# Kernel optimization log

Measured on AMD Instinct MI355X. Metric: run time of the kernel, lower is better.

## Reference

```python
import jax, jax.numpy as jnp
import numpy as np

TAU_M, TAU_S = 4.0, 1.0
EM = float(np.exp(-1.0 / TAU_M))  # membrane decay exp(-1/tau_m)
ES = float(np.exp(-1.0 / TAU_S))  # synapse decay exp(-1/tau_s)
V_TH = 1.0


@jax.custom_vjp
def spike(v):
    # Heaviside spike with rectangular surrogate gradient (snn-iir style)
    return (v >= V_TH).astype(v.dtype)

def _spike_fwd(v):
    return spike(v), v

def _spike_bwd(v, g):
    return (g * (jnp.abs(v - V_TH) < 0.5).astype(g.dtype),)

spike.defvjp(_spike_fwd, _spike_bwd)


def dual_exp_iir(x, em, es):
    # dual-exponential synaptic filter as two coupled first-order IIRs
    # x: [B, F, T] -> y: [B, F, T]
    xT = jnp.moveaxis(x, -1, 0)  # [T, B, F]
    def step(carry, xt):
        m, s = carry
        m = em * m + xt
        s = es * s + xt
        return (m, s), m - s
    z = jnp.zeros_like(xT[0])
    _, y = jax.lax.scan(step, (z, z), xT)
    return jnp.moveaxis(y, 0, -1)


def lif_layer(x, w, b, decay):
    # Linear then LIF neuron with hard reset and membrane filter
    # x: [B, I, T], w: [O, I], b: [O] -> spikes: [B, O, T]
    wx = jnp.einsum('bit,oi->tbo', x, w) + b  # [T, B, O]
    def step(carry, cur):
        v, sp = carry
        v = decay * v * (1.0 - sp) + cur
        sp = spike(v)
        return (v, sp), sp
    z = jnp.zeros(wx.shape[1:], wx.dtype)
    _, spikes = jax.lax.scan(step, (z, z), wx)
    return jnp.moveaxis(spikes, 0, -1)


def setup_inputs() -> dict:
    key = jax.random.key(0)
    ks = jax.random.split(key, 8)
    B, T, F = 64, 512, 500
    inputs = jax.random.uniform(ks[0], (B, 784, T), jnp.float32)
    eps = jax.random.normal(ks[1], (B, F, T), jnp.float32)
    w1 = jax.random.normal(ks[2], (1000, 784), jnp.float32) * (1.0 / np.sqrt(784.0))
    b1 = jax.random.normal(ks[3], (1000,), jnp.float32) * 0.01
    w2 = jax.random.normal(ks[4], (500, 500), jnp.float32) * (1.0 / np.sqrt(500.0))
    b2 = jax.random.normal(ks[5], (500,), jnp.float32) * 0.01
    w3 = jax.random.normal(ks[6], (10, 500), jnp.float32) * (1.0 / np.sqrt(500.0))
    b3 = jax.random.normal(ks[7], (10,), jnp.float32) * 0.01
    return dict(inputs=inputs, eps=eps, w1=w1, b1=b1, w2=w2, b2=b2, w3=w3, b3=b3)


def reference(inputs, eps, w1, b1, w2, b2, w3, b3):
    F = 500
    # ANN encoder applied independently per timestep (steady_state)
    ann = jax.nn.relu(jnp.einsum('bit,oi->bot', inputs, w1) + b1[None, :, None])  # [B,1000,T]
    mu = ann[:, :F, :]
    ln_var = ann[:, F:, :]
    sample = mu + eps * jnp.exp(0.5 * ln_var)  # VAE reparameterization, [B,500,T]
    a2 = dual_exp_iir(sample, EM, ES)
    s2 = lif_layer(a2, w2, b2, EM)
    a3 = dual_exp_iir(s2, EM, ES)
    s3 = lif_layer(a3, w3, b3, EM)  # [B,10,T]
    return s3
```

## Files before the change

### kernel.cpp

```cpp
#include <hip/hip_runtime.h>

#define EMD 0.77880078307140486824
#define ESD 0.36787944117144232160
#define TCG 256
#define TCS 128

typedef double d4 __attribute__((ext_vector_type(4)));

__global__ void mfma_probe(double* __restrict__ flagOut)
{
    const int lane = threadIdx.x & 63;
    const int lr = lane & 15;
    const int lk = lane >> 4;
    const double a = 100.0 * lr + lk + 1.0;
    const double b = 1000.0 * lk + lr + 7.0;
    d4 c = {};
    c = __builtin_amdgcn_mfma_f64_16x16x4f64(a, b, c, 0, 0, 0);
    int myflag = 4;
    for (int h = 3; h >= 0; --h) {
        int ok = 1;
        for (int v = 0; v < 4; ++v) {
            int i, j;
            if (h == 0)      { i = 4 * lk + v; j = lr; }
            else if (h == 1) { i = lk + 4 * v; j = lr; }
            else if (h == 2) { i = lr; j = 4 * lk + v; }
            else             { i = lr; j = lk + 4 * v; }
            double e = 0.0;
            for (int k = 0; k < 4; ++k)
                e += (100.0 * i + k + 1.0) * (1000.0 * k + j + 7.0);
            if (c[v] != e) ok = 0;
        }
        if (__all(ok)) myflag = h;
    }
    if (lane == 0) flagOut[0] = (double)myflag;
}

__device__ __forceinline__ void frag_rc(int flag, int lk, int lr, int v,
                                        int& rl, int& cl)
{
    if (flag == 1)      { rl = lk + 4 * v; cl = lr; }
    else if (flag == 2) { rl = lr; cl = 4 * lk + v; }
    else if (flag == 3) { rl = lr; cl = lk + 4 * v; }
    else                { rl = 4 * lk + v; cl = lr; }
}

__global__ __launch_bounds__(256) void g1_mfma(
    const float* __restrict__ X,
    const float* __restrict__ W1,
    const float* __restrict__ B1,
    const float* __restrict__ EPS,
    double* __restrict__ SAMP,
    const double* __restrict__ FLG,
    int t0)
{
    const int b   = blockIdx.z;
    const int m0  = blockIdx.y * 64;
    const int tt0 = blockIdx.x * 64;
    const int tg  = t0 + tt0;

    __shared__ float Am[16][68];
    __shared__ float Al[16][68];
    __shared__ float Bs[16][68];

    const int tid  = threadIdx.x;
    const int lane = tid & 63;
    const int wid  = tid >> 6;
    const int wf   = (wid >> 1) * 32;
    const int wt   = (wid & 1) * 32;
    const int lr   = lane & 15;
    const int lk   = lane >> 4;

    d4 accm[2][2] = {};
    d4 accl[2][2] = {};

    for (int k0 = 0; k0 < 784; k0 += 16) {
        {
            const int m  = tid >> 2;
            const int kk = (tid & 3) * 4;
            int f = m0 + m; if (f > 499) f = 499;
            const float4 aw = *(const float4*)&W1[(size_t)f * 784 + k0 + kk];
            Am[kk+0][m] = aw.x; Am[kk+1][m] = aw.y;
            Am[kk+2][m] = aw.z; Am[kk+3][m] = aw.w;
            const float4 lw = *(const float4*)&W1[(size_t)(500 + f) * 784 + k0 + kk];
            Al[kk+0][m] = lw.x; Al[kk+1][m] = lw.y;
            Al[kk+2][m] = lw.z; Al[kk+3][m] = lw.w;
        }
        {
            const int bk = tid >> 4;
            const int bt = (tid & 15) * 4;
            *(float4*)&Bs[bk][bt] =
                *(const float4*)&X[((size_t)b * 784 + k0 + bk) * 512 + tg + bt];
        }
        __syncthreads();
        #pragma unroll
        for (int ks = 0; ks < 4; ++ks) {
            const int kr = 4 * ks + lk;
            const double a0 = (double)Am[kr][wf + lr];
            const double a1 = (double)Am[kr][wf + 16 + lr];
            const double l0 = (double)Al[kr][wf + lr];
            const double l1 = (double)Al[kr][wf + 16 + lr];
            const double b0 = (double)Bs[kr][wt + lr];
            const double b1 = (double)Bs[kr][wt + 16 + lr];
            accm[0][0] = __builtin_amdgcn_mfma_f64_16x16x4f64(a0, b0, accm[0][0], 0, 0, 0);
            accm[0][1] = __builtin_amdgcn_mfma_f64_16x16x4f64(a0, b1, accm[0][1], 0, 0, 0);
            accm[1][0] = __builtin_amdgcn_mfma_f64_16x16x4f64(a1, b0, accm[1][0], 0, 0, 0);
            accm[1][1] = __builtin_amdgcn_mfma_f64_16x16x4f64(a1, b1, accm[1][1], 0, 0, 0);
            accl[0][0] = __builtin_amdgcn_mfma_f64_16x16x4f64(l0, b0, accl[0][0], 0, 0, 0);
            accl[0][1] = __builtin_amdgcn_mfma_f64_16x16x4f64(l0, b1, accl[0][1], 0, 0, 0);
            accl[1][0] = __builtin_amdgcn_mfma_f64_16x16x4f64(l1, b0, accl[1][0], 0, 0, 0);
            accl[1][1] = __builtin_amdgcn_mfma_f64_16x16x4f64(l1, b1, accl[1][1], 0, 0, 0);
        }
        __syncthreads();
    }

    const int flag = (int)FLG[0];
    for (int fi = 0; fi < 2; ++fi)
    for (int tj = 0; tj < 2; ++tj)
    for (int v = 0; v < 4; ++v) {
        int rl, cl;
        frag_rc(flag, lk, lr, v, rl, cl);
        const int f = m0 + wf + fi * 16 + rl;
        if (f >= 500) continue;
        const int tloc = tt0 + wt + tj * 16 + cl;
        const double bm = (double)B1[f];
        const double bl = (double)B1[500 + f];
        const double mu = fmax(accm[fi][tj][v] + bm, 0.0);
        const double lv = fmax(accl[fi][tj][v] + bl, 0.0);
        const double e  = (double)EPS[((size_t)b * 500 + f) * 512 + t0 + tloc];
        SAMP[((size_t)b * 500 + f) * TCG + tloc] = mu + e * exp(0.5 * lv);
    }
}

__global__ __launch_bounds__(256) void iir2_chunk(
    double* __restrict__ A,
    double* __restrict__ stM, double* __restrict__ stS, int first)
{
    __shared__ double tile[64][65];
    const int tid = threadIdx.x;
    const int r0 = blockIdx.x * 64;
    double m = 0.0, s = 0.0;
    if (tid < 64 && !first) { m = stM[r0 + tid]; s = stS[r0 + tid]; }

    for (int sub = 0; sub < TCG / 64; ++sub) {
        #pragma unroll
        for (int q = 0; q < 8; ++q) {
            const int e2 = q * 256 + tid;
            const int r = e2 >> 5;
            const int c = (e2 & 31) * 2;
            const double2 v = *(const double2*)&A[(size_t)(r0 + r) * TCG + sub * 64 + c];
            tile[r][c] = v.x; tile[r][c + 1] = v.y;
        }
        __syncthreads();
        if (tid < 64) {
            #pragma unroll
            for (int c = 0; c < 64; ++c) {
                const double x = tile[tid][c];
                m = EMD * m + x;
                s = ESD * s + x;
                tile[tid][c] = m - s;
            }
        }
        __syncthreads();
        #pragma unroll
        for (int q = 0; q < 8; ++q) {
            const int e2 = q * 256 + tid;
            const int r = e2 >> 5;
            const int c = (e2 & 31) * 2;
            double2 v; v.x = tile[r][c]; v.y = tile[r][c + 1];
            *(double2*)&A[(size_t)(r0 + r) * TCG + sub * 64 + c] = v;
        }
        __syncthreads();
    }
    if (tid < 64) { stM[r0 + tid] = m; stS[r0 + tid] = s; }
}

__global__ __launch_bounds__(256) void g2_mfma(
    const double* __restrict__ A2,
    const float* __restrict__ W2,
    const float* __restrict__ B2,
    double* __restrict__ WX2,
    const double* __restrict__ FLG,
    int t_off)
{
    const int b   = blockIdx.z;
    const int o0  = blockIdx.y * 64;
    const int tl0 = blockIdx.x * 64;

    __shared__ double At[16][66];
    __shared__ float  Wo[16][68];

    const int tid  = threadIdx.x;
    const int lane = tid & 63;
    const int wid  = tid >> 6;
    const int wtl  = (wid >> 1) * 32;
    const int wo   = (wid & 1) * 32;
    const int lr   = lane & 15;
    const int lk   = lane >> 4;

    d4 acc[2][2] = {};

    for (int k0 = 0; k0 < 512; k0 += 16) {
        {
            const int kk = tid >> 4;
            const int t4 = (tid & 15) * 4;
            const int f = k0 + kk;
            if (f < 500) {
                const size_t base = ((size_t)b * 500 + f) * TCG + t_off + tl0 + t4;
                const double2 v0 = *(const double2*)&A2[base];
                const double2 v1 = *(const double2*)&A2[base + 2];
                At[kk][t4+0] = v0.x; At[kk][t4+1] = v0.y;
                At[kk][t4+2] = v1.x; At[kk][t4+3] = v1.y;
            } else {
                At[kk][t4+0] = 0.0; At[kk][t4+1] = 0.0;
                At[kk][t4+2] = 0.0; At[kk][t4+3] = 0.0;
            }
        }
        {
            const int oo = tid >> 2;
            const int fc = (tid & 3) * 4;
            int o = o0 + oo; if (o > 499) o = 499;
            const int f = k0 + fc;
            if (f + 3 < 500) {
                const float4 w = *(const float4*)&W2[(size_t)o * 500 + f];
                Wo[fc+0][oo] = w.x; Wo[fc+1][oo] = w.y;
                Wo[fc+2][oo] = w.z; Wo[fc+3][oo] = w.w;
            } else {
                #pragma unroll
                for (int c = 0; c < 4; ++c)
                    Wo[fc+c][oo] = (f + c < 500) ? W2[(size_t)o * 500 + f + c] : 0.0f;
            }
        }
        __syncthreads();
        #pragma unroll
        for (int ks = 0; ks < 4; ++ks) {
            const int kr = 4 * ks + lk;
            const double a0 = At[kr][wtl + lr];
            const double a1 = At[kr][wtl + 16 + lr];
            const double w0 = (double)Wo[kr][wo + lr];
            const double w1 = (double)Wo[kr][wo + 16 + lr];
            acc[0][0] = __builtin_amdgcn_mfma_f64_16x16x4f64(a0, w0, acc[0][0], 0, 0, 0);
            acc[0][1] = __builtin_amdgcn_mfma_f64_16x16x4f64(a0, w1, acc[0][1], 0, 0, 0);
            acc[1][0] = __builtin_amdgcn_mfma_f64_16x16x4f64(a1, w0, acc[1][0], 0, 0, 0);
            acc[1][1] = __builtin_amdgcn_mfma_f64_16x16x4f64(a1, w1, acc[1][1], 0, 0, 0);
        }
        __syncthreads();
    }

    const int flag = (int)FLG[0];
    for (int ti = 0; ti < 2; ++ti)
    for (int oj = 0; oj < 2; ++oj)
    for (int v = 0; v < 4; ++v) {
        int rl, cl;
        frag_rc(flag, lk, lr, v, rl, cl);
        const int tl = tl0 + wtl + ti * 16 + rl;
        const int o  = o0 + wo + oj * 16 + cl;
        if (o < 500)
            WX2[((size_t)tl * 64 + b) * 500 + o] = acc[ti][oj][v] + (double)B2[o];
    }
}

__global__ __launch_bounds__(256) void lif2iir3_chunk(
    double* __restrict__ WX,
    double* __restrict__ stV, double* __restrict__ stSp,
    double* __restrict__ stM, double* __restrict__ stS, int first)
{
    const int idx = blockIdx.x * 256 + threadIdx.x;
    if (idx >= 32000) return;
    double v, sp, m, s;
    if (first) { v = 0.0; sp = 0.0; m = 0.0; s = 0.0; }
    else { v = stV[idx]; sp = stSp[idx]; m = stM[idx]; s = stS[idx]; }
    for (int tt = 0; tt < TCS; ++tt) {
        const double cur = WX[(size_t)tt * 32000 + idx];
        v = EMD * v * (1.0 - sp) + cur;
        sp = (v >= 1.0) ? 1.0 : 0.0;
        m = EMD * m + sp;
        s = ESD * s + sp;
        WX[(size_t)tt * 32000 + idx] = m - s;
    }
    stV[idx] = v; stSp[idx] = sp; stM[idx] = m; stS[idx] = s;
}

__global__ __launch_bounds__(256) void g3_chunk(
    const double* __restrict__ A3,
    const float* __restrict__ W3,
    const float* __restrict__ B3,
    double* __restrict__ WX3)
{
    __shared__ float w3s[5000];
    for (int i = threadIdx.x; i < 5000; i += 256) w3s[i] = W3[i];
    __syncthreads();

    const int lane = threadIdx.x & 63;
    const int R = blockIdx.x * 4 + (threadIdx.x >> 6);
    const double* row = A3 + (size_t)R * 500;

    double p[10] = {};
    #pragma unroll
    for (int c = 0; c < 8; ++c) {
        const int i = c * 64 + lane;
        const int ii = (i < 500) ? i : 0;
        const double x = (i < 500) ? row[ii] : 0.0;
        #pragma unroll
        for (int o = 0; o < 10; ++o)
            p[o] = fma(x, (double)w3s[o * 500 + ii], p[o]);
    }
    #pragma unroll
    for (int off = 32; off; off >>= 1)
        #pragma unroll
        for (int o = 0; o < 10; ++o)
            p[o] += __shfl_xor(p[o], off, 64);
    if (lane < 10)
        WX3[(size_t)R * 10 + lane] = p[lane] + (double)B3[lane];
}

__global__ __launch_bounds__(256) void lif3_chunk(
    const double* __restrict__ WX3, float* __restrict__ OUT,
    double* __restrict__ stV, double* __restrict__ stSp, int first, int t0)
{
    const int idx = blockIdx.x * 256 + threadIdx.x;
    if (idx >= 640) return;
    double v = first ? 0.0 : stV[idx];
    double sp = first ? 0.0 : stSp[idx];
    for (int tt = 0; tt < TCS; ++tt) {
        const double cur = WX3[(size_t)tt * 640 + idx];
        v = EMD * v * (1.0 - sp) + cur;
        sp = (v >= 1.0) ? 1.0 : 0.0;
        OUT[(size_t)idx * 512 + t0 + tt] = (float)sp;
    }
    stV[idx] = v; stSp[idx] = sp;
}

__global__ void sent_kernel(float* __restrict__ OUT, float v) { OUT[0] = v; }

extern "C" void kernel_launch(void* const* d_in, const int* in_sizes, int n_in,
                              void* d_out, int out_size, void* d_ws, size_t ws_size,
                              hipStream_t stream)
{
    float* OUT = (float*)d_out;

    const int expect[8] = {25690112, 16384000, 784000, 1000, 250000, 500, 5000, 10};
    int bad = -1;
    if (n_in != 8) bad = 0;
    else {
        for (int k = 0; k < 8; ++k)
            if (in_sizes[k] != expect[k]) { bad = 1 + k; break; }
        if (bad < 0 && out_size != 327680) bad = 9;
        if (bad < 0 && ws_size < (size_t)131072000) bad = 10;
    }
    if (bad >= 0) {
        sent_kernel<<<1, 1, 0, stream>>>(OUT, 4100.0f + bad);
        return;
    }

    const float* X   = (const float*)d_in[0];
    const float* EPS = (const float*)d_in[1];
    const float* W1  = (const float*)d_in[2];
    const float* B1  = (const float*)d_in[3];
    const float* W2  = (const float*)d_in[4];
    const float* B2  = (const float*)d_in[5];
    const float* W3  = (const float*)d_in[6];
    const float* B3  = (const float*)d_in[7];

    double* ws = (double*)d_ws;
    double* buf1  = ws;
    double* buf2  = ws + 8192000;
    double* buf4  = ws + 12288000;
    double* stM2  = ws + 12400000;
    double* stS2  = ws + 12432000;
    double* stV2  = ws + 12464000;
    double* stSp2 = ws + 12496000;
    double* stM3  = ws + 12528000;
    double* stS3  = ws + 12560000;
    double* stV3  = ws + 12592000;
    double* stSp3 = ws + 12593000;
    double* FLG   = ws + 12600000;

    mfma_probe<<<1, 64, 0, stream>>>(FLG);

    for (int tc = 0; tc < 512 / TCG; ++tc) {
        const int t0 = tc * TCG;
        const int firstc = (tc == 0) ? 1 : 0;
        g1_mfma<<<dim3(TCG / 64, 8, 64), 256, 0, stream>>>(X, W1, B1, EPS, buf1, FLG, t0);
        iir2_chunk<<<500, 256, 0, stream>>>(buf1, stM2, stS2, firstc);
        for (int h = 0; h < TCG / TCS; ++h) {
            const int first = (firstc && h == 0) ? 1 : 0;
            g2_mfma<<<dim3(TCS / 64, 8, 64), 256, 0, stream>>>(buf1, W2, B2, buf2, FLG, h * TCS);
            lif2iir3_chunk<<<125, 256, 0, stream>>>(buf2, stV2, stSp2, stM3, stS3, first);
            g3_chunk<<<2048, 256, 0, stream>>>(buf2, W3, B3, buf4);
            lif3_chunk<<<3, 256, 0, stream>>>(buf4, OUT, stV3, stSp3, first, t0 + h * TCS);
        }
    }
}
```

Measured before the change: 1.682 ms.

## Double-buffer shared tiles and enlarge per-warp tiles in FP64 MFMA GEMMs

```diff
diff --git a/kernel.cpp b/kernel.cpp
--- a/kernel.cpp
+++ b/kernel.cpp
@@ -55,77 +55,100 @@
 {
     const int b   = blockIdx.z;
     const int m0  = blockIdx.y * 64;
-    const int tt0 = blockIdx.x * 64;
+    const int tt0 = blockIdx.x * 128;
     const int tg  = t0 + tt0;
 
-    __shared__ float Am[16][68];
-    __shared__ float Al[16][68];
-    __shared__ float Bs[16][68];
+    __shared__ float Am[2][16][80];
+    __shared__ float Al[2][16][80];
+    __shared__ float Bs[2][16][136];
 
     const int tid  = threadIdx.x;
     const int lane = tid & 63;
     const int wid  = tid >> 6;
     const int wf   = (wid >> 1) * 32;
-    const int wt   = (wid & 1) * 32;
+    const int wt   = (wid & 1) * 64;
     const int lr   = lane & 15;
     const int lk   = lane >> 4;
 
-    d4 accm[2][2] = {};
-    d4 accl[2][2] = {};
-
-    for (int k0 = 0; k0 < 784; k0 += 16) {
-        {
-            const int m  = tid >> 2;
-            const int kk = (tid & 3) * 4;
-            int f = m0 + m; if (f > 499) f = 499;
-            const float4 aw = *(const float4*)&W1[(size_t)f * 784 + k0 + kk];
-            Am[kk+0][m] = aw.x; Am[kk+1][m] = aw.y;
-            Am[kk+2][m] = aw.z; Am[kk+3][m] = aw.w;
-            const float4 lw = *(const float4*)&W1[(size_t)(500 + f) * 784 + k0 + kk];
-            Al[kk+0][m] = lw.x; Al[kk+1][m] = lw.y;
-            Al[kk+2][m] = lw.z; Al[kk+3][m] = lw.w;
-        }
-        {
-            const int bk = tid >> 4;
-            const int bt = (tid & 15) * 4;
-            *(float4*)&Bs[bk][bt] =
-                *(const float4*)&X[((size_t)b * 784 + k0 + bk) * 512 + tg + bt];
-        }
-        __syncthreads();
+    const int sm  = tid >> 2;
+    const int skk = (tid & 3) * 4;
+    int sf = m0 + sm; if (sf > 499) sf = 499;
+    const float* wa_ptr = &W1[(size_t)sf * 784 + skk];
+    const float* wl_ptr = &W1[(size_t)(500 + sf) * 784 + skk];
+    const int sbk = tid >> 4;
+    const int sbt = (tid & 15) * 8;
+    const float* x_ptr = &X[((size_t)b * 784 + sbk) * 512 + tg + sbt];
+
+    d4 accm[2][4] = {};
+    d4 accl[2][4] = {};
+
+    {
+        const float4 aw = *(const float4*)wa_ptr;
+        const float4 lw = *(const float4*)wl_ptr;
+        Am[0][skk+0][sm] = aw.x; Am[0][skk+1][sm] = aw.y;
+        Am[0][skk+2][sm] = aw.z; Am[0][skk+3][sm] = aw.w;
+        Al[0][skk+0][sm] = lw.x; Al[0][skk+1][sm] = lw.y;
+        Al[0][skk+2][sm] = lw.z; Al[0][skk+3][sm] = lw.w;
+        *(float4*)&Bs[0][sbk][sbt]     = *(const float4*)x_ptr;
+        *(float4*)&Bs[0][sbk][sbt + 4] = *(const float4*)(x_ptr + 4);
+    }
+    __syncthreads();
+
+    for (int it = 0; it < 49; ++it) {
+        const int cur = it & 1;
+        float4 aw, lw, x0, x1;
+        if (it < 48) {
+            const int ko = (it + 1) * 16;
+            aw = *(const float4*)(wa_ptr + ko);
+            lw = *(const float4*)(wl_ptr + ko);
+            x0 = *(const float4*)(x_ptr + (size_t)ko * 512);
+            x1 = *(const float4*)(x_ptr + (size_t)ko * 512 + 4);
+        }
         #pragma unroll
         for (int ks = 0; ks < 4; ++ks) {
             const int kr = 4 * ks + lk;
-            const double a0 = (double)Am[kr][wf + lr];
-            const double a1 = (double)Am[kr][wf + 16 + lr];
-            const double l0 = (double)Al[kr][wf + lr];
-            const double l1 = (double)Al[kr][wf + 16 + lr];
-            const double b0 = (double)Bs[kr][wt + lr];
-            const double b1 = (double)Bs[kr][wt + 16 + lr];
-            accm[0][0] = __builtin_amdgcn_mfma_f64_16x16x4f64(a0, b0, accm[0][0], 0, 0, 0);
-            accm[0][1] = __builtin_amdgcn_mfma_f64_16x16x4f64(a0, b1, accm[0][1], 0, 0, 0);
-            accm[1][0] = __builtin_amdgcn_mfma_f64_16x16x4f64(a1, b0, accm[1][0], 0, 0, 0);
-            accm[1][1] = __builtin_amdgcn_mfma_f64_16x16x4f64(a1, b1, accm[1][1], 0, 0, 0);
-            accl[0][0] = __builtin_amdgcn_mfma_f64_16x16x4f64(l0, b0, accl[0][0], 0, 0, 0);
-            accl[0][1] = __builtin_amdgcn_mfma_f64_16x16x4f64(l0, b1, accl[0][1], 0, 0, 0);
-            accl[1][0] = __builtin_amdgcn_mfma_f64_16x16x4f64(l1, b0, accl[1][0], 0, 0, 0);
-            accl[1][1] = __builtin_amdgcn_mfma_f64_16x16x4f64(l1, b1, accl[1][1], 0, 0, 0);
+            const double a0 = (double)Am[cur][kr][wf + lr];
+            const double a1 = (double)Am[cur][kr][wf + 16 + lr];
+            const double l0 = (double)Al[cur][kr][wf + lr];
+            const double l1 = (double)Al[cur][kr][wf + 16 + lr];
+            double bb[4];
+            #pragma unroll
+            for (int h = 0; h < 4; ++h)
+                bb[h] = (double)Bs[cur][kr][wt + 16 * h + lr];
+            #pragma unroll
+            for (int h = 0; h < 4; ++h) {
+                accm[0][h] = __builtin_amdgcn_mfma_f64_16x16x4f64(a0, bb[h], accm[0][h], 0, 0, 0);
+                accm[1][h] = __builtin_amdgcn_mfma_f64_16x16x4f64(a1, bb[h], accm[1][h], 0, 0, 0);
+                accl[0][h] = __builtin_amdgcn_mfma_f64_16x16x4f64(l0, bb[h], accl[0][h], 0, 0, 0);
+                accl[1][h] = __builtin_amdgcn_mfma_f64_16x16x4f64(l1, bb[h], accl[1][h], 0, 0, 0);
+            }
+        }
+        __syncthreads();
+        if (it < 48) {
+            const int nxt = cur ^ 1;
+            Am[nxt][skk+0][sm] = aw.x; Am[nxt][skk+1][sm] = aw.y;
+            Am[nxt][skk+2][sm] = aw.z; Am[nxt][skk+3][sm] = aw.w;
+            Al[nxt][skk+0][sm] = lw.x; Al[nxt][skk+1][sm] = lw.y;
+            Al[nxt][skk+2][sm] = lw.z; Al[nxt][skk+3][sm] = lw.w;
+            *(float4*)&Bs[nxt][sbk][sbt]     = x0;
+            *(float4*)&Bs[nxt][sbk][sbt + 4] = x1;
         }
         __syncthreads();
     }
 
     const int flag = (int)FLG[0];
     for (int fi = 0; fi < 2; ++fi)
-    for (int tj = 0; tj < 2; ++tj)
+    for (int h = 0; h < 4; ++h)
     for (int v = 0; v < 4; ++v) {
         int rl, cl;
         frag_rc(flag, lk, lr, v, rl, cl);
         const int f = m0 + wf + fi * 16 + rl;
         if (f >= 500) continue;
-        const int tloc = tt0 + wt + tj * 16 + cl;
+        const int tloc = tt0 + wt + h * 16 + cl;
         const double bm = (double)B1[f];
         const double bl = (double)B1[500 + f];
-        const double mu = fmax(accm[fi][tj][v] + bm, 0.0);
-        const double lv = fmax(accl[fi][tj][v] + bl, 0.0);
+        const double mu = fmax(accm[fi][h][v] + bm, 0.0);
+        const double lv = fmax(accl[fi][h][v] + bl, 0.0);
         const double e  = (double)EPS[((size_t)b * 500 + f) * 512 + t0 + tloc];
         SAMP[((size_t)b * 500 + f) * TCG + tloc] = mu + e * exp(0.5 * lv);
     }
@@ -183,79 +206,102 @@
     int t_off)
 {
     const int b   = blockIdx.z;
-    const int o0  = blockIdx.y * 64;
+    const int o0  = blockIdx.y * 128;
     const int tl0 = blockIdx.x * 64;
 
-    __shared__ double At[16][66];
-    __shared__ float  Wo[16][68];
+    __shared__ double At[2][16][72];
+    __shared__ float  Wo[2][16][136];
 
     const int tid  = threadIdx.x;
     const int lane = tid & 63;
     const int wid  = tid >> 6;
     const int wtl  = (wid >> 1) * 32;
-    const int wo   = (wid & 1) * 32;
+    const int wo   = (wid & 1) * 64;
     const int lr   = lane & 15;
     const int lk   = lane >> 4;
 
-    d4 acc[2][2] = {};
-
-    for (int k0 = 0; k0 < 512; k0 += 16) {
-        {
-            const int kk = tid >> 4;
-            const int t4 = (tid & 15) * 4;
-            const int f = k0 + kk;
-            if (f < 500) {
-                const size_t base = ((size_t)b * 500 + f) * TCG + t_off + tl0 + t4;
-                const double2 v0 = *(const double2*)&A2[base];
-                const double2 v1 = *(const double2*)&A2[base + 2];
-                At[kk][t4+0] = v0.x; At[kk][t4+1] = v0.y;
-                At[kk][t4+2] = v1.x; At[kk][t4+3] = v1.y;
-            } else {
-                At[kk][t4+0] = 0.0; At[kk][t4+1] = 0.0;
-                At[kk][t4+2] = 0.0; At[kk][t4+3] = 0.0;
-            }
-        }
-        {
-            const int oo = tid >> 2;
-            const int fc = (tid & 3) * 4;
-            int o = o0 + oo; if (o > 499) o = 499;
-            const int f = k0 + fc;
-            if (f + 3 < 500) {
-                const float4 w = *(const float4*)&W2[(size_t)o * 500 + f];
-                Wo[fc+0][oo] = w.x; Wo[fc+1][oo] = w.y;
-                Wo[fc+2][oo] = w.z; Wo[fc+3][oo] = w.w;
+    const int akk = tid >> 4;
+    const int at4 = (tid & 15) * 4;
+    const double* a_ptr = &A2[((size_t)b * 500 + akk) * TCG + t_off + tl0 + at4];
+    const int woo = tid & 127;
+    const int wfc = (tid >> 7) * 8;
+    int so = o0 + woo; if (so > 499) so = 499;
+    const float* w_ptr = &W2[(size_t)so * 500 + wfc];
+
+    d4 acc[2][4] = {};
+
+    {
+        const double2 v0 = *(const double2*)a_ptr;
+        const double2 v1 = *(const double2*)(a_ptr + 2);
+        *(double2*)&At[0][akk][at4]     = v0;
+        *(double2*)&At[0][akk][at4 + 2] = v1;
+        const float4 w0 = *(const float4*)w_ptr;
+        const float4 w1 = *(const float4*)(w_ptr + 4);
+        Wo[0][wfc+0][woo] = w0.x; Wo[0][wfc+1][woo] = w0.y;
+        Wo[0][wfc+2][woo] = w0.z; Wo[0][wfc+3][woo] = w0.w;
+        Wo[0][wfc+4][woo] = w1.x; Wo[0][wfc+5][woo] = w1.y;
+        Wo[0][wfc+6][woo] = w1.z; Wo[0][wfc+7][woo] = w1.w;
+    }
+    __syncthreads();
+
+    for (int it = 0; it < 32; ++it) {
+        const int cur = it & 1;
+        double2 v0, v1; float wr[8];
+        if (it < 31) {
+            const int k0n = (it + 1) * 16;
+            if (k0n + akk < 500) {
+                v0 = *(const double2*)(a_ptr + (size_t)k0n * TCG);
+                v1 = *(const double2*)(a_ptr + (size_t)k0n * TCG + 2);
+            } else { v0.x = v0.y = v1.x = v1.y = 0.0; }
+            if (k0n + wfc + 7 < 500) {
+                const float4 w0 = *(const float4*)(w_ptr + k0n);
+                const float4 w1 = *(const float4*)(w_ptr + k0n + 4);
+                wr[0]=w0.x; wr[1]=w0.y; wr[2]=w0.z; wr[3]=w0.w;
+                wr[4]=w1.x; wr[5]=w1.y; wr[6]=w1.z; wr[7]=w1.w;
             } else {
                 #pragma unroll
-                for (int c = 0; c < 4; ++c)
-                    Wo[fc+c][oo] = (f + c < 500) ? W2[(size_t)o * 500 + f + c] : 0.0f;
+                for (int c = 0; c < 8; ++c)
+                    wr[c] = (k0n + wfc + c < 500) ? w_ptr[k0n + c] : 0.0f;
             }
         }
-        __syncthreads();
         #pragma unroll
         for (int ks = 0; ks < 4; ++ks) {
             const int kr = 4 * ks + lk;
-            const double a0 = At[kr][wtl + lr];
-            const double a1 = At[kr][wtl + 16 + lr];
-            const double w0 = (double)Wo[kr][wo + lr];
-            const double w1 = (double)Wo[kr][wo + 16 + lr];
-            acc[0][0] = __builtin_amdgcn_mfma_f64_16x16x4f64(a0, w0, acc[0][0], 0, 0, 0);
-            acc[0][1] = __builtin_amdgcn_mfma_f64_16x16x4f64(a0, w1, acc[0][1], 0, 0, 0);
-            acc[1][0] = __builtin_amdgcn_mfma_f64_16x16x4f64(a1, w0, acc[1][0], 0, 0, 0);
-            acc[1][1] = __builtin_amdgcn_mfma_f64_16x16x4f64(a1, w1, acc[1][1], 0, 0, 0);
+            const double a0 = At[cur][kr][wtl + lr];
+            const double a1 = At[cur][kr][wtl + 16 + lr];
+            double ww[4];
+            #pragma unroll
+            for (int h = 0; h < 4; ++h)
+                ww[h] = (double)Wo[cur][kr][wo + 16 * h + lr];
+            #pragma unroll
+            for (int h = 0; h < 4; ++h) {
+                acc[0][h] = __builtin_amdgcn_mfma_f64_16x16x4f64(a0, ww[h], acc[0][h], 0, 0, 0);
+                acc[1][h] = __builtin_amdgcn_mfma_f64_16x16x4f64(a1, ww[h], acc[1][h], 0, 0, 0);
+            }
+        }
+        __syncthreads();
+        if (it < 31) {
+            const int nxt = cur ^ 1;
+            *(double2*)&At[nxt][akk][at4]     = v0;
+            *(double2*)&At[nxt][akk][at4 + 2] = v1;
+            Wo[nxt][wfc+0][woo] = wr[0]; Wo[nxt][wfc+1][woo] = wr[1];
+            Wo[nxt][wfc+2][woo] = wr[2]; Wo[nxt][wfc+3][woo] = wr[3];
+            Wo[nxt][wfc+4][woo] = wr[4]; Wo[nxt][wfc+5][woo] = wr[5];
+            Wo[nxt][wfc+6][woo] = wr[6]; Wo[nxt][wfc+7][woo] = wr[7];
         }
         __syncthreads();
     }
 
     const int flag = (int)FLG[0];
-    for (int ti = 0; ti < 2; ++ti)
-    for (int oj = 0; oj < 2; ++oj)
+    for (int fi = 0; fi < 2; ++fi)
+    for (int h = 0; h < 4; ++h)
     for (int v = 0; v < 4; ++v) {
         int rl, cl;
         frag_rc(flag, lk, lr, v, rl, cl);
-        const int tl = tl0 + wtl + ti * 16 + rl;
-        const int o  = o0 + wo + oj * 16 + cl;
+        const int tl = tl0 + wtl + fi * 16 + rl;
+        const int o  = o0 + wo + h * 16 + cl;
         if (o < 500)
-            WX2[((size_t)tl * 64 + b) * 500 + o] = acc[ti][oj][v] + (double)B2[o];
+            WX2[((size_t)tl * 64 + b) * 500 + o] = acc[fi][h][v] + (double)B2[o];
     }
 }
 
@@ -380,11 +426,11 @@
     for (int tc = 0; tc < 512 / TCG; ++tc) {
         const int t0 = tc * TCG;
         const int firstc = (tc == 0) ? 1 : 0;
-        g1_mfma<<<dim3(TCG / 64, 8, 64), 256, 0, stream>>>(X, W1, B1, EPS, buf1, FLG, t0);
+        g1_mfma<<<dim3(TCG / 128, 8, 64), 256, 0, stream>>>(X, W1, B1, EPS, buf1, FLG, t0);
         iir2_chunk<<<500, 256, 0, stream>>>(buf1, stM2, stS2, firstc);
         for (int h = 0; h < TCG / TCS; ++h) {
             const int first = (firstc && h == 0) ? 1 : 0;
-            g2_mfma<<<dim3(TCS / 64, 8, 64), 256, 0, stream>>>(buf1, W2, B2, buf2, FLG, h * TCS);
+            g2_mfma<<<dim3(TCS / 64, 4, 64), 256, 0, stream>>>(buf1, W2, B2, buf2, FLG, h * TCS);
             lif2iir3_chunk<<<125, 256, 0, stream>>>(buf2, stV2, stSp2, stM3, stS3, first);
             g3_chunk<<<2048, 256, 0, stream>>>(buf2, W3, B3, buf4);
             lif3_chunk<<<3, 256, 0, stream>>>(buf4, OUT, stV3, stSp3, first, t0 + h * TCS);
```

After: 4.666 ms. 2.77x slower.
